# Kernel optimization log

Hardware: AMD Instinct MI355X
Metric: run time of the kernel (lower is better)

Reference implementation:

```python
import jax, jax.numpy as jnp
import numpy as np

DIM = 1024
NUM_HEADS = 16
HEAD_DIM = DIM // NUM_HEADS
B, N = 4, 2048


def _rope_sin_cos(seq_len, head_dim, dtype=jnp.float32):
    inv_freq = 1.0 / (10000.0 ** (jnp.arange(0, head_dim, 2, dtype=jnp.float32) / head_dim))
    t = jnp.arange(seq_len, dtype=jnp.float32)
    freqs = jnp.einsum('i,j->ij', t, inv_freq)          # [N, head_dim/2]
    emb = jnp.concatenate([freqs, freqs], axis=-1)      # [N, head_dim]
    return jnp.sin(emb).astype(dtype), jnp.cos(emb).astype(dtype)


def _rotate_half(x):
    x1, x2 = jnp.split(x, 2, axis=-1)
    return jnp.concatenate([-x2, x1], axis=-1)


def setup_inputs() -> dict:
    key = jax.random.key(0)
    k1, k2, k3, k4, k5 = jax.random.split(key, 5)
    scale = 0.02
    return {
        'x': jax.random.normal(k1, (B, N, DIM), dtype=jnp.float32),
        'W_qkv': jax.random.normal(k2, (DIM, 3 * DIM), dtype=jnp.float32) * scale,
        'b_qkv': jax.random.normal(k3, (3 * DIM,), dtype=jnp.float32) * scale,
        'W_proj': jax.random.normal(k4, (DIM, DIM), dtype=jnp.float32) * scale,
        'b_proj': jax.random.normal(k5, (DIM,), dtype=jnp.float32) * scale,
    }


def reference(x, W_qkv, b_qkv, W_proj, b_proj):
    Bsz, Nlen, C = x.shape
    H, Dh = NUM_HEADS, HEAD_DIM
    qkv = x @ W_qkv + b_qkv                              # [B, N, 3C]
    q, k, v = jnp.split(qkv, 3, axis=-1)
    # [B, H, N, Dh]
    q = q.reshape(Bsz, Nlen, H, Dh).transpose(0, 2, 1, 3)
    k = k.reshape(Bsz, Nlen, H, Dh).transpose(0, 2, 1, 3)
    v = v.reshape(Bsz, Nlen, H, Dh).transpose(0, 2, 1, 3)
    sin, cos = _rope_sin_cos(Nlen, Dh, x.dtype)          # [N, Dh] each, broadcast
    q = q * cos + _rotate_half(q) * sin
    k = k * cos + _rotate_half(k) * sin
    scale = 1.0 / jnp.sqrt(jnp.asarray(Dh, x.dtype))
    scores = jnp.einsum('bhqd,bhkd->bhqk', q, k) * scale  # [B, H, N, N]
    attn = jax.nn.softmax(scores, axis=-1)
    out = jnp.einsum('bhqk,bhkd->bhqd', attn, v)          # [B, H, N, Dh]
    out = out.transpose(0, 2, 1, 3).reshape(Bsz, Nlen, C)
    return out @ W_proj + b_proj
```

## Files before the change

### kernel.cpp

```cpp
#include <hip/hip_runtime.h>
#include <hip/hip_bf16.h>
#include <math.h>

#define BSZ 4
#define NSEQ 2048
#define CDIM 1024
#define NH 16
#define DH 64
#define KC 64
#define KMAX_STRIDE 32

typedef _Float16 half8_t __attribute__((ext_vector_type(8)));
typedef _Float16 half4_t __attribute__((ext_vector_type(4)));
typedef __fp16 pk2_t __attribute__((ext_vector_type(2)));
typedef __fp16 pk4_t __attribute__((ext_vector_type(4)));
typedef float floatx4 __attribute__((ext_vector_type(4)));

#define GLOBAL_AS(p) ((const __attribute__((address_space(1))) void*)(p))
#define LDS_AS(p)    ((__attribute__((address_space(3))) void*)(p))

__global__ __launch_bounds__(256) void cast_x_kernel(
    const float* __restrict__ src, _Float16* __restrict__ dst) {
  const size_t i = ((size_t)blockIdx.x * 256 + threadIdx.x) * 8;
  float4 a = *(const float4*)(src + i);
  float4 b = *(const float4*)(src + i + 4);
  half8_t h;
  h[0] = (_Float16)a.x; h[1] = (_Float16)a.y; h[2] = (_Float16)a.z; h[3] = (_Float16)a.w;
  h[4] = (_Float16)b.x; h[5] = (_Float16)b.y; h[6] = (_Float16)b.z; h[7] = (_Float16)b.w;
  *(half8_t*)(dst + i) = h;
}

__global__ __launch_bounds__(256) void transpose_cast_kernel(
    const float* __restrict__ src, _Float16* __restrict__ dst, int R, int C) {
  __shared__ float Ls[64][65];
  const int t = threadIdx.x;
  const int r0 = blockIdx.y * 64, c0 = blockIdx.x * 64;
  {
    const int lr = t >> 2, lcg = (t & 3) * 16;
    const float* s = src + (size_t)(r0 + lr) * C + c0 + lcg;
#pragma unroll
    for (int u = 0; u < 4; ++u)
      *(float4*)&Ls[lr][lcg + 4 * u] = *(const float4*)(s + 4 * u);
  }
  __syncthreads();
  const int c = t >> 2, rg = (t & 3) * 16;
  half8_t h0, h1;
#pragma unroll
  for (int u = 0; u < 8; ++u) h0[u] = (_Float16)Ls[rg + u][c];
#pragma unroll
  for (int u = 0; u < 8; ++u) h1[u] = (_Float16)Ls[rg + 8 + u][c];
  _Float16* d = dst + (size_t)(c0 + c) * R + r0 + rg;
  *(half8_t*)d = h0;
  *(half8_t*)(d + 8) = h1;
}

__global__ __launch_bounds__(256) void qkv_gemm_kernel(
    const _Float16* __restrict__ xh, const _Float16* __restrict__ Wt,
    const float* __restrict__ bias, _Float16* __restrict__ Qh,
    _Float16* __restrict__ Kh, _Float16* __restrict__ Vh) {
  __shared__ _Float16 As[128 * 64];
  __shared__ _Float16 Bs[128 * 64];
  const int tid = threadIdx.x;
  const int lane = tid & 63, w = tid >> 6;
  const int m = lane & 15, quad = lane >> 4;
  const int wr = (w >> 1) * 64, wc = (w & 1) * 64;
  const int m0 = blockIdx.y * 128;
  const int N0 = blockIdx.x * 128;
  const int sr = lane >> 3, sc = (lane & 7) * 8;

  floatx4 acc[4][4];
#pragma unroll
  for (int i = 0; i < 4; ++i)
#pragma unroll
    for (int j = 0; j < 4; ++j) acc[i][j] = (floatx4){0.f, 0.f, 0.f, 0.f};

  for (int k0 = 0; k0 < CDIM; k0 += 64) {
    __syncthreads();
#pragma unroll
    for (int i = 0; i < 4; ++i) {
      const int row = (w * 4 + i) * 8 + sr;
      __builtin_amdgcn_global_load_lds(
          GLOBAL_AS(xh + (size_t)(m0 + row) * CDIM + k0 + sc),
          LDS_AS(As + (w * 4 + i) * 512), 16, 0, 0);
      __builtin_amdgcn_global_load_lds(
          GLOBAL_AS(Wt + (size_t)(N0 + row) * CDIM + k0 + sc),
          LDS_AS(Bs + (w * 4 + i) * 512), 16, 0, 0);
    }
    __syncthreads();
#pragma unroll
    for (int ks = 0; ks < 2; ++ks) {
      half8_t af[4], bf[4];
#pragma unroll
      for (int mt = 0; mt < 4; ++mt)
        af[mt] = *(half8_t*)(As + (wr + mt * 16 + m) * 64 + ks * 32 + quad * 8);
#pragma unroll
      for (int nt = 0; nt < 4; ++nt)
        bf[nt] = *(half8_t*)(Bs + (wc + nt * 16 + m) * 64 + ks * 32 + quad * 8);
#pragma unroll
      for (int mt = 0; mt < 4; ++mt)
#pragma unroll
        for (int nt = 0; nt < 4; ++nt)
          acc[mt][nt] = __builtin_amdgcn_mfma_f32_16x16x32_f16(
              af[mt], bf[nt], acc[mt][nt], 0, 0, 0);
    }
  }

  const int F0 = N0 + wc;
  const int which = F0 >> 10;
  const int head = (F0 & 1023) >> 6;
  float bv[4];
#pragma unroll
  for (int nt = 0; nt < 4; ++nt) bv[nt] = bias[F0 + nt * 16 + m];

  if (which == 2) {
#pragma unroll
    for (int mt = 0; mt < 4; ++mt)
#pragma unroll
      for (int reg = 0; reg < 4; ++reg) {
        const int gm = m0 + wr + mt * 16 + 4 * quad + reg;
        const int b = gm >> 11, n = gm & 2047;
        const size_t vbase = ((size_t)(b * NH + head) * DH) * NSEQ + n;
#pragma unroll
        for (int nt = 0; nt < 4; ++nt)
          Vh[vbase + (size_t)(nt * 16 + m) * NSEQ] =
              (_Float16)(acc[mt][nt][reg] + bv[nt]);
      }
  } else {
    _Float16* dst = which ? Kh : Qh;
    const float qs = which ? 1.0f : 0.125f * 1.4426950408889634f;
    const float invfA = expf(-9.210340371976184f * ((float)m * (1.0f / 32.0f)));
    const float invfB = expf(-9.210340371976184f * ((float)(16 + m) * (1.0f / 32.0f)));
#pragma unroll
    for (int mt = 0; mt < 4; ++mt)
#pragma unroll
      for (int reg = 0; reg < 4; ++reg) {
        const int gm = m0 + wr + mt * 16 + 4 * quad + reg;
        const int b = gm >> 11, n = gm & 2047;
        float sA, cA, sB, cB;
        sincosf((float)n * invfA, &sA, &cA);
        sincosf((float)n * invfB, &sB, &cB);
        const size_t obase = ((size_t)(b * NH + head) * NSEQ + n) * DH;
#pragma unroll
        for (int nt = 0; nt < 4; ++nt) {
          const float val = acc[mt][nt][reg] + bv[nt];
          const float rot = (nt < 2) ? -(acc[mt][nt + 2][reg] + bv[nt + 2])
                                     :  (acc[mt][nt - 2][reg] + bv[nt - 2]);
          const float sv = (nt & 1) ? sB : sA;
          const float cv = (nt & 1) ? cB : cA;
          dst[obase + nt * 16 + m] = (_Float16)((val * cv + rot * sv) * qs);
        }
      }
  }
}

__global__ __launch_bounds__(64) void kmax_init_kernel(unsigned* kmaxu) {
  for (int i = threadIdx.x; i < 64 * KMAX_STRIDE; i += 64) kmaxu[i] = 0u;
}

__global__ __launch_bounds__(256) void qk_norms_kernel(
    const _Float16* __restrict__ Qh, const _Float16* __restrict__ Kh,
    float* __restrict__ qn, unsigned* __restrict__ kmaxu) {
  __shared__ float wmax[4];
  const int tid = threadIdx.x;
  const size_t row = (size_t)blockIdx.x * 32 + (tid >> 3);
  const int c = (tid & 7) * 8;
  half8_t q8 = *(const half8_t*)(Qh + row * DH + c);
  half8_t k8 = *(const half8_t*)(Kh + row * DH + c);
  float qs = 0.f, ks = 0.f;
#pragma unroll
  for (int u = 0; u < 8; ++u) {
    const float qv = (float)q8[u], kv = (float)k8[u];
    qs += qv * qv; ks += kv * kv;
  }
  qs += __shfl_xor(qs, 1, 64); ks += __shfl_xor(ks, 1, 64);
  qs += __shfl_xor(qs, 2, 64); ks += __shfl_xor(ks, 2, 64);
  qs += __shfl_xor(qs, 4, 64); ks += __shfl_xor(ks, 4, 64);
  if ((tid & 7) == 0) qn[row] = sqrtf(qs);
  ks = fmaxf(ks, __shfl_xor(ks, 8, 64));
  ks = fmaxf(ks, __shfl_xor(ks, 16, 64));
  ks = fmaxf(ks, __shfl_xor(ks, 32, 64));
  if ((tid & 63) == 0) wmax[tid >> 6] = ks;
  __syncthreads();
  if (tid == 0) {
    const float mx = fmaxf(fmaxf(wmax[0], wmax[1]), fmaxf(wmax[2], wmax[3]));
    atomicMax(&kmaxu[(row >> 11) * KMAX_STRIDE], __float_as_uint(sqrtf(mx)));
  }
}

__global__ __launch_bounds__(256) void attn_kernel(
    const _Float16* __restrict__ Qh, const _Float16* __restrict__ Kh,
    const _Float16* __restrict__ Vh, const float* __restrict__ qn,
    const unsigned* __restrict__ kmaxu, _Float16* __restrict__ AO) {
  __shared__ char smem[18432];
  _Float16* Ks = (_Float16*)smem;
  _Float16* Vt = (_Float16*)(smem + 9216);
  float* Os = (float*)smem;

  const int tid = threadIdx.x;
  const int lane = tid & 63;
  const int w = tid >> 6;
  const int m = lane & 15;
  const int quad = lane >> 4;
  const int bh = blockIdx.y;
  const int q0 = blockIdx.x * 128;

  const _Float16* Qb = Qh + (size_t)bh * NSEQ * DH;
  const _Float16* Kb = Kh + (size_t)bh * NSEQ * DH;
  const _Float16* Vb = Vh + (size_t)bh * DH * NSEQ;

  const int rA = q0 + w * 32 + m;
  const int rB = rA + 16;
  half8_t qfA0 = *(const half8_t*)(Qb + (size_t)rA * DH + quad * 8);
  half8_t qfA1 = *(const half8_t*)(Qb + (size_t)rA * DH + 32 + quad * 8);
  half8_t qfB0 = *(const half8_t*)(Qb + (size_t)rB * DH + quad * 8);
  half8_t qfB1 = *(const half8_t*)(Qb + (size_t)rB * DH + 32 + quad * 8);

  const float kmx = __uint_as_float(kmaxu[bh * KMAX_STRIDE]);
  const float mA = qn[(size_t)bh * NSEQ + rA] * kmx;
  const float mB = qn[(size_t)bh * NSEQ + rB] * kmx;

  const int skey = tid >> 3, sdg = (tid & 7) * 8;
  const _Float16* ksrc0 = Kb + (size_t)skey * DH + sdg;
  const _Float16* ksrc1 = Kb + (size_t)(skey + 32) * DH + sdg;
  const _Float16* vsrc0 = Vb + (size_t)skey * NSEQ + sdg;
  const _Float16* vsrc1 = Vb + (size_t)(skey + 32) * NSEQ + sdg;
  _Float16* kdst0 = Ks + skey * 72 + sdg;
  _Float16* kdst1 = Ks + (skey + 32) * 72 + sdg;
  _Float16* vdst0 = Vt + skey * 72 + sdg;
  _Float16* vdst1 = Vt + (skey + 32) * 72 + sdg;

  float lA = 0.f, lB = 0.f;
  floatx4 OA[4], OB[4];
#pragma unroll
  for (int nb = 0; nb < 4; ++nb) {
    OA[nb] = (floatx4){0.f, 0.f, 0.f, 0.f};
    OB[nb] = (floatx4){0.f, 0.f, 0.f, 0.f};
  }
  const pk2_t one2 = {(__fp16)1.f, (__fp16)1.f};

  for (int ck = 0; ck < NSEQ / KC; ++ck) {
    __syncthreads();
    *(half8_t*)kdst0 = *(const half8_t*)ksrc0;  ksrc0 += KC * DH;
    *(half8_t*)kdst1 = *(const half8_t*)ksrc1;  ksrc1 += KC * DH;
    *(half8_t*)vdst0 = *(const half8_t*)vsrc0;  vsrc0 += KC;
    *(half8_t*)vdst1 = *(const half8_t*)vsrc1;  vsrc1 += KC;
    __syncthreads();

#pragma unroll
    for (int kt = 0; kt < 4; ++kt) {
      half8_t kf0 = *(half8_t*)(Ks + (kt * 16 + m) * 72 + quad * 8);
      half8_t kf1 = *(half8_t*)(Ks + (kt * 16 + m) * 72 + 32 + quad * 8);
      floatx4 a = (floatx4){-mA, -mA, -mA, -mA};
      a = __builtin_amdgcn_mfma_f32_16x16x32_f16(kf0, qfA0, a, 0, 0, 0);
      a = __builtin_amdgcn_mfma_f32_16x16x32_f16(kf1, qfA1, a, 0, 0, 0);
      floatx4 b = (floatx4){-mB, -mB, -mB, -mB};
      b = __builtin_amdgcn_mfma_f32_16x16x32_f16(kf0, qfB0, b, 0, 0, 0);
      b = __builtin_amdgcn_mfma_f32_16x16x32_f16(kf1, qfB1, b, 0, 0, 0);

      const float pA0 = __builtin_exp2f(a[0]);
      const float pA1 = __builtin_exp2f(a[1]);
      const float pA2 = __builtin_exp2f(a[2]);
      const float pA3 = __builtin_exp2f(a[3]);
      const float pB0 = __builtin_exp2f(b[0]);
      const float pB1 = __builtin_exp2f(b[1]);
      const float pB2 = __builtin_exp2f(b[2]);
      const float pB3 = __builtin_exp2f(b[3]);
      pk2_t a01 = __builtin_amdgcn_cvt_pkrtz(pA0, pA1);
      pk2_t a23 = __builtin_amdgcn_cvt_pkrtz(pA2, pA3);
      pk2_t b01 = __builtin_amdgcn_cvt_pkrtz(pB0, pB1);
      pk2_t b23 = __builtin_amdgcn_cvt_pkrtz(pB2, pB3);
      lA = __builtin_amdgcn_fdot2(a01, one2, lA, false);
      lA = __builtin_amdgcn_fdot2(a23, one2, lA, false);
      lB = __builtin_amdgcn_fdot2(b01, one2, lB, false);
      lB = __builtin_amdgcn_fdot2(b23, one2, lB, false);
      half4_t phA = __builtin_bit_cast(
          half4_t, (pk4_t)__builtin_shufflevector(a01, a23, 0, 1, 2, 3));
      half4_t phB = __builtin_bit_cast(
          half4_t, (pk4_t)__builtin_shufflevector(b01, b23, 0, 1, 2, 3));

#pragma unroll
      for (int nb = 0; nb < 4; ++nb) {
        half4_t vf = *(half4_t*)(Vt + (nb * 16 + m) * 72 + kt * 16 + quad * 4);
        OA[nb] = __builtin_amdgcn_mfma_f32_16x16x16f16(phA, vf, OA[nb], 0, 0, 0);
        OB[nb] = __builtin_amdgcn_mfma_f32_16x16x16f16(phB, vf, OB[nb], 0, 0, 0);
      }
    }
  }

  lA += __shfl_xor(lA, 16, 64); lA += __shfl_xor(lA, 32, 64);
  lB += __shfl_xor(lB, 16, 64); lB += __shfl_xor(lB, 32, 64);
  float lA4[4], lB4[4];
#pragma unroll
  for (int r = 0; r < 4; ++r) {
    lA4[r] = __shfl(lA, 4 * quad + r, 64);
    lB4[r] = __shfl(lB, 4 * quad + r, 64);
  }

  const int b = bh >> 4, h = bh & 15;
  const int ql = tid >> 2, dgo = (tid & 3) * 16;
  const int gq = q0 + (ql >> 4) * 32 + (ql & 15);
  _Float16* dstA = AO + ((size_t)(b * NSEQ + gq)) * CDIM + h * DH + dgo;

  __syncthreads();
#pragma unroll
  for (int nb = 0; nb < 4; ++nb)
#pragma unroll
    for (int r = 0; r < 4; ++r)
      Os[(w * 16 + 4 * quad + r) * 68 + nb * 16 + m] = OA[nb][r] * (1.0f / lA4[r]);
  __syncthreads();
#pragma unroll
  for (int u = 0; u < 2; ++u) {
    half8_t o;
#pragma unroll
    for (int v = 0; v < 8; ++v) o[v] = (_Float16)Os[ql * 68 + dgo + u * 8 + v];
    *(half8_t*)(dstA + u * 8) = o;
  }

  __syncthreads();
#pragma unroll
  for (int nb = 0; nb < 4; ++nb)
#pragma unroll
    for (int r = 0; r < 4; ++r)
      Os[(w * 16 + 4 * quad + r) * 68 + nb * 16 + m] = OB[nb][r] * (1.0f / lB4[r]);
  __syncthreads();
  _Float16* dstB = dstA + (size_t)16 * CDIM;
#pragma unroll
  for (int u = 0; u < 2; ++u) {
    half8_t o;
#pragma unroll
    for (int v = 0; v < 8; ++v) o[v] = (_Float16)Os[ql * 68 + dgo + u * 8 + v];
    *(half8_t*)(dstB + u * 8) = o;
  }
}

__global__ __launch_bounds__(256) void proj_gemm_kernel(
    const _Float16* __restrict__ Ah, const _Float16* __restrict__ Wt,
    const float* __restrict__ bias, float* __restrict__ out) {
  __shared__ _Float16 As[128 * 64];
  __shared__ _Float16 Bs[128 * 64];
  const int tid = threadIdx.x;
  const int lane = tid & 63, w = tid >> 6;
  const int m = lane & 15, quad = lane >> 4;
  const int wr = (w >> 1) * 64, wc = (w & 1) * 64;
  const int m0 = blockIdx.y * 128;
  const int N0 = blockIdx.x * 128;
  const int sr = lane >> 3, sc = (lane & 7) * 8;

  floatx4 acc[4][4];
#pragma unroll
  for (int i = 0; i < 4; ++i)
#pragma unroll
    for (int j = 0; j < 4; ++j) acc[i][j] = (floatx4){0.f, 0.f, 0.f, 0.f};

  for (int k0 = 0; k0 < CDIM; k0 += 64) {
    __syncthreads();
#pragma unroll
    for (int i = 0; i < 4; ++i) {
      const int row = (w * 4 + i) * 8 + sr;
      __builtin_amdgcn_global_load_lds(
          GLOBAL_AS(Ah + (size_t)(m0 + row) * CDIM + k0 + sc),
          LDS_AS(As + (w * 4 + i) * 512), 16, 0, 0);
      __builtin_amdgcn_global_load_lds(
          GLOBAL_AS(Wt + (size_t)(N0 + row) * CDIM + k0 + sc),
          LDS_AS(Bs + (w * 4 + i) * 512), 16, 0, 0);
    }
    __syncthreads();
#pragma unroll
    for (int ks = 0; ks < 2; ++ks) {
      half8_t af[4], bf[4];
#pragma unroll
      for (int mt = 0; mt < 4; ++mt)
        af[mt] = *(half8_t*)(As + (wr + mt * 16 + m) * 64 + ks * 32 + quad * 8);
#pragma unroll
      for (int nt = 0; nt < 4; ++nt)
        bf[nt] = *(half8_t*)(Bs + (wc + nt * 16 + m) * 64 + ks * 32 + quad * 8);
#pragma unroll
      for (int mt = 0; mt < 4; ++mt)
#pragma unroll
        for (int nt = 0; nt < 4; ++nt)
          acc[mt][nt] = __builtin_amdgcn_mfma_f32_16x16x32_f16(
              af[mt], bf[nt], acc[mt][nt], 0, 0, 0);
    }
  }

  const int F0 = N0 + wc;
  float bv[4];
#pragma unroll
  for (int nt = 0; nt < 4; ++nt) bv[nt] = bias[F0 + nt * 16 + m];
#pragma unroll
  for (int mt = 0; mt < 4; ++mt)
#pragma unroll
    for (int reg = 0; reg < 4; ++reg) {
      const int gm = m0 + wr + mt * 16 + 4 * quad + reg;
#pragma unroll
      for (int nt = 0; nt < 4; ++nt)
        out[(size_t)gm * CDIM + F0 + nt * 16 + m] = acc[mt][nt][reg] + bv[nt];
    }
}

extern "C" void kernel_launch(void* const* d_in, const int* in_sizes, int n_in,
                              void* d_out, int out_size, void* d_ws, size_t ws_size,
                              hipStream_t stream) {
  const float* x     = (const float*)d_in[0];
  const float* Wqkv  = (const float*)d_in[1];
  const float* bqkv  = (const float*)d_in[2];
  const float* Wproj = (const float*)d_in[3];
  const float* bproj = (const float*)d_in[4];
  float* out = (float*)d_out;

  const size_t per = (size_t)BSZ * NH * NSEQ * DH;
  _Float16* xh  = (_Float16*)d_ws;
  _Float16* Wt  = xh + per;
  _Float16* Wpt = Wt + (size_t)3072 * 1024;
  _Float16* Qh  = Wpt + (size_t)1024 * 1024;
  _Float16* Kh  = Qh + per;
  _Float16* Vh  = Kh + per;
  _Float16* AOh = Vh + per;
  float*    qnp = (float*)(AOh + per);
  unsigned* kmx = (unsigned*)(qnp + (size_t)64 * NSEQ);

  cast_x_kernel<<<4096, 256, 0, stream>>>(x, xh);
  transpose_cast_kernel<<<dim3(48, 16), 256, 0, stream>>>(Wqkv, Wt, 1024, 3072);
  transpose_cast_kernel<<<dim3(16, 16), 256, 0, stream>>>(Wproj, Wpt, 1024, 1024);
  kmax_init_kernel<<<1, 64, 0, stream>>>(kmx);
  qkv_gemm_kernel<<<dim3(24, 64), 256, 0, stream>>>(xh, Wt, bqkv, Qh, Kh, Vh);
  qk_norms_kernel<<<4096, 256, 0, stream>>>(Qh, Kh, qnp, kmx);
  attn_kernel<<<dim3(16, 64), 256, 0, stream>>>(Qh, Kh, Vh, qnp, kmx, AOh);
  proj_gemm_kernel<<<dim3(8, 64), 256, 0, stream>>>(AOh, Wpt, bproj, out);
}
```

Baseline: 351.0 us.

## Double-buffer K/V tiles in LDS with register prefetch and MFMA priority hints

The attention loop now prefetches the next K/V chunk into registers and writes it to an alternate LDS buffer while the current buffer is consumed. This removes one barrier per iteration and hides global-load latency behind MFMA work. It also wraps the MFMA groups in s_setprio so matrix issue is favoured over other waves. The cost is doubled LDS use (36 KB) and extra live registers, which may lower occupancy.

```diff
diff --git a/kernel.cpp b/kernel.cpp
--- a/kernel.cpp
+++ b/kernel.cpp
@@ -191,9 +191,7 @@
     const _Float16* __restrict__ Qh, const _Float16* __restrict__ Kh,
     const _Float16* __restrict__ Vh, const float* __restrict__ qn,
     const unsigned* __restrict__ kmaxu, _Float16* __restrict__ AO) {
-  __shared__ char smem[18432];
-  _Float16* Ks = (_Float16*)smem;
-  _Float16* Vt = (_Float16*)(smem + 9216);
+  __shared__ _Float16 smem[18432];
   float* Os = (float*)smem;
 
   const int tid = threadIdx.x;
@@ -224,10 +222,24 @@
   const _Float16* ksrc1 = Kb + (size_t)(skey + 32) * DH + sdg;
   const _Float16* vsrc0 = Vb + (size_t)skey * NSEQ + sdg;
   const _Float16* vsrc1 = Vb + (size_t)(skey + 32) * NSEQ + sdg;
-  _Float16* kdst0 = Ks + skey * 72 + sdg;
-  _Float16* kdst1 = Ks + (skey + 32) * 72 + sdg;
-  _Float16* vdst0 = Vt + skey * 72 + sdg;
-  _Float16* vdst1 = Vt + (skey + 32) * 72 + sdg;
+  const int koff0 = skey * 72 + sdg;
+  const int koff1 = (skey + 32) * 72 + sdg;
+
+  half8_t rk0, rk1, rv0, rv1;
+  auto LOAD = [&]() {
+    rk0 = *(const half8_t*)ksrc0; ksrc0 += KC * DH;
+    rk1 = *(const half8_t*)ksrc1; ksrc1 += KC * DH;
+    rv0 = *(const half8_t*)vsrc0; vsrc0 += KC;
+    rv1 = *(const half8_t*)vsrc1; vsrc1 += KC;
+  };
+  auto WRITE = [&](int boff) {
+    _Float16* Ksb = smem + boff;
+    _Float16* Vtb = smem + boff + 4608;
+    *(half8_t*)(Ksb + koff0) = rk0;
+    *(half8_t*)(Ksb + koff1) = rk1;
+    *(half8_t*)(Vtb + koff0) = rv0;
+    *(half8_t*)(Vtb + koff1) = rv1;
+  };
 
   float lA = 0.f, lB = 0.f;
   floatx4 OA[4], OB[4];
@@ -238,24 +250,21 @@
   }
   const pk2_t one2 = {(__fp16)1.f, (__fp16)1.f};
 
-  for (int ck = 0; ck < NSEQ / KC; ++ck) {
-    __syncthreads();
-    *(half8_t*)kdst0 = *(const half8_t*)ksrc0;  ksrc0 += KC * DH;
-    *(half8_t*)kdst1 = *(const half8_t*)ksrc1;  ksrc1 += KC * DH;
-    *(half8_t*)vdst0 = *(const half8_t*)vsrc0;  vsrc0 += KC;
-    *(half8_t*)vdst1 = *(const half8_t*)vsrc1;  vsrc1 += KC;
-    __syncthreads();
-
+  auto COMPUTE = [&](int boff) {
+    _Float16* Ks = smem + boff;
+    _Float16* Vt = smem + boff + 4608;
 #pragma unroll
     for (int kt = 0; kt < 4; ++kt) {
       half8_t kf0 = *(half8_t*)(Ks + (kt * 16 + m) * 72 + quad * 8);
       half8_t kf1 = *(half8_t*)(Ks + (kt * 16 + m) * 72 + 32 + quad * 8);
+      __builtin_amdgcn_s_setprio(1);
       floatx4 a = (floatx4){-mA, -mA, -mA, -mA};
       a = __builtin_amdgcn_mfma_f32_16x16x32_f16(kf0, qfA0, a, 0, 0, 0);
       a = __builtin_amdgcn_mfma_f32_16x16x32_f16(kf1, qfA1, a, 0, 0, 0);
       floatx4 b = (floatx4){-mB, -mB, -mB, -mB};
       b = __builtin_amdgcn_mfma_f32_16x16x32_f16(kf0, qfB0, b, 0, 0, 0);
       b = __builtin_amdgcn_mfma_f32_16x16x32_f16(kf1, qfB1, b, 0, 0, 0);
+      __builtin_amdgcn_s_setprio(0);
 
       const float pA0 = __builtin_exp2f(a[0]);
       const float pA1 = __builtin_exp2f(a[1]);
@@ -278,12 +287,28 @@
       half4_t phB = __builtin_bit_cast(
           half4_t, (pk4_t)__builtin_shufflevector(b01, b23, 0, 1, 2, 3));
 
+      __builtin_amdgcn_s_setprio(1);
 #pragma unroll
       for (int nb = 0; nb < 4; ++nb) {
         half4_t vf = *(half4_t*)(Vt + (nb * 16 + m) * 72 + kt * 16 + quad * 4);
         OA[nb] = __builtin_amdgcn_mfma_f32_16x16x16f16(phA, vf, OA[nb], 0, 0, 0);
         OB[nb] = __builtin_amdgcn_mfma_f32_16x16x16f16(phB, vf, OB[nb], 0, 0, 0);
       }
+      __builtin_amdgcn_s_setprio(0);
+    }
+  };
+
+  LOAD();
+  WRITE(0);
+  LOAD();
+
+  const int NCK = NSEQ / KC;
+  for (int ck = 0; ck < NCK; ++ck) {
+    __syncthreads();
+    COMPUTE((ck & 1) * 9216);
+    if (ck + 1 < NCK) {
+      WRITE(((ck + 1) & 1) * 9216);
+      if (ck + 2 < NCK) LOAD();
     }
   }
 
```

Result: faster. 340.1 us (-3.1%).
